# Performance work log

Hardware: AMD Instinct MI355X
Metric: run time of the kernel (lower is better)

## Reference

```python
import jax, jax.numpy as jnp
import numpy as np

# ---- sign binarization with straight-through estimator (standard BNN) ----
@jax.custom_vjp
def binarize(x):
    return jnp.where(x >= 0, 1.0, -1.0).astype(x.dtype)

def _bin_fwd(x):
    return binarize(x), x

def _bin_bwd(x, g):
    return (g * (jnp.abs(x) <= 1.0).astype(g.dtype),)

binarize.defvjp(_bin_fwd, _bin_bwd)

def conv2d(x, w):
    # x: [N,C,H,W], w: [O,I,kh,kw], stride 1, VALID padding (padding=0)
    return jax.lax.conv_general_dilated(
        x, w, window_strides=(1, 1), padding='VALID',
        dimension_numbers=('NCHW', 'OIHW', 'NCHW'))

def maxpool2(x):
    return jax.lax.reduce_window(x, -jnp.inf, jax.lax.max,
                                 (1, 1, 2, 2), (1, 1, 2, 2), 'VALID')

def hardtanh(x):
    return jnp.clip(x, -1.0, 1.0)

def setup_inputs() -> dict:
    key = jax.random.key(0)
    ks = jax.random.split(key, 11)
    B = 8192
    s = 0.1
    return {
        'x':   jax.random.normal(ks[0], (B, 3, 32, 32), jnp.float32),
        'w1':  jax.random.normal(ks[1], (6, 3, 5, 5), jnp.float32) * s,
        'b1':  jax.random.normal(ks[2], (6,), jnp.float32) * s,
        'w2':  jax.random.normal(ks[3], (16, 6, 5, 5), jnp.float32) * s,
        'b2':  jax.random.normal(ks[4], (16,), jnp.float32) * s,
        'wf1': jax.random.normal(ks[5], (120, 400), jnp.float32) * s,
        'bf1': jax.random.normal(ks[6], (120,), jnp.float32) * s,
        'wf2': jax.random.normal(ks[7], (84, 120), jnp.float32) * s,
        'bf2': jax.random.normal(ks[8], (84,), jnp.float32) * s,
        'wf3': jax.random.normal(ks[9], (10, 84), jnp.float32) * s,
        'bf3': jax.random.normal(ks[10], (10,), jnp.float32) * s,
    }

def reference(x, w1, b1, w2, b2, wf1, bf1, wf2, bf2, wf3, bf3):
    # conv1: first layer -> real-valued input, binarized weights
    out = conv2d(x, binarize(w1)) + b1[None, :, None, None]   # [B,6,28,28]
    out = maxpool2(hardtanh(out))                              # [B,6,14,14]
    # conv2: binarized input and weights
    out = conv2d(binarize(out), binarize(w2)) + b2[None, :, None, None]  # [B,16,10,10]
    out = maxpool2(hardtanh(out))                              # [B,16,5,5]
    out = out.reshape(out.shape[0], -1)                        # [B,400]
    out = hardtanh(binarize(out) @ binarize(wf1).T + bf1)      # [B,120]
    out = hardtanh(binarize(out) @ binarize(wf2).T + bf2)      # [B,84]
    out = binarize(out) @ binarize(wf3).T + bf3                # [B,10]
    return out
```

## Files before the change

kernel.cpp:

```cpp
#include <hip/hip_runtime.h>
#include <stdint.h>

#define TPB 64
#define RCAP 64
#define BAND 0.05f

#define WS_BFR   0
#define WS_W1B   1280
#define WS_W2PK  1298
#define WS_WF1P  1378
#define WS_WF2PK 4380
#define WS_WF3PK 4716
#define WS_T2    4746
#define WS_TF1   4762
#define WS_TF2   4882

typedef _Float16 half8 __attribute__((ext_vector_type(8)));
typedef float f32x4 __attribute__((ext_vector_type(4)));
typedef unsigned int u32x4 __attribute__((ext_vector_type(4)));

__device__ __forceinline__ uint32_t pkf16(float a, float b) {
  uint32_t lo = (uint32_t)__builtin_bit_cast(uint16_t, (_Float16)a);
  uint32_t hi = (uint32_t)__builtin_bit_cast(uint16_t, (_Float16)b);
  return lo | (hi << 16);
}

__device__ __forceinline__ float qpswap(float v) {
  return __builtin_bit_cast(float, __builtin_amdgcn_mov_dpp(
      __builtin_bit_cast(int, v), 0xB1, 0xF, 0xF, true));
}

__device__ __forceinline__ double win_sum(const float* __restrict__ xb,
                                          uint32_t b0, uint32_t b1, uint32_t b2) {
  double s = 0.0;
#pragma unroll
  for (int ic = 0; ic < 3; ++ic)
#pragma unroll
    for (int rr = 0; rr < 5; ++rr) {
      const float* rp = xb + ic * 1024 + rr * 32;
#pragma unroll
      for (int kc = 0; kc < 5; ++kc) {
        const int idx = ic * 25 + rr * 5 + kc;
        const uint32_t bw = (idx < 32) ? b0 : ((idx < 64) ? b1 : b2);
        double xv = (double)rp[kc];
        s += ((bw >> (idx & 31)) & 1u) ? xv : -xv;
      }
    }
  return s;
}

__global__ __launch_bounds__(256) void prep_kernel(
    const float* __restrict__ w1, const float* __restrict__ w2,
    const float* __restrict__ wf1, const float* __restrict__ wf2,
    const float* __restrict__ wf3,
    const float* __restrict__ b2, const float* __restrict__ bf1,
    const float* __restrict__ bf2, uint32_t* __restrict__ wsu)
{
  int id = blockIdx.x * 256 + threadIdx.x;
  if (id < 1280) {
    int s = id >> 8, r = id & 255, ln = r >> 2, dw = r & 3;
    int g4 = ln >> 4, n = ln & 15;
    int o = 4 * s + g4, r6 = o / 3, cp = o % 3;
    int c = n >> 1, dy = n & 1;
    uint32_t w = 0;
    for (int h = 0; h < 2; ++h) {
      int j2 = dw * 2 + h;
      int ic = j2 & 3, pix = j2 >> 2, kc = cp * 2 + pix, kr = r6 - dy;
      uint32_t f = 0;
      if (n < 12 && o < 18 && ic < 3 && kc < 5 && kr >= 0 && kr <= 4)
        f = (w1[(c * 3 + ic) * 25 + kr * 5 + kc] >= 0.f) ? 0x3C00u : 0xBC00u;
      w |= f << (16 * h);
    }
    wsu[WS_BFR + id] = w;
  } else if (id < 1298) {
    int i = id - 1280, c = i / 3, q = i % 3;
    uint32_t w = 0;
    for (int b = 0; b < 32; ++b) {
      int k = q * 32 + b;
      if (k < 75) w |= (uint32_t)(w1[c*75 + k] >= 0.f) << b;
    }
    wsu[WS_W1B + i] = w;
  } else if (id < 1378) {
    int r = id - 1298, oc = r / 5, kr = r % 5;
    uint32_t w = 0;
    for (int c = 0; c < 6; ++c)
      for (int k = 0; k < 5; ++k)
        w |= (uint32_t)(w2[((oc*6 + c)*5 + kr)*5 + k] >= 0.f) << (5*c + k);
    wsu[WS_W2PK + r] = w;
  } else if (id < 4378) {
    int r = id - 1378, o = r / 25, p = r % 25;
    uint32_t w = 0;
    for (int oc = 0; oc < 16; ++oc)
      w |= (uint32_t)(wf1[o*400 + oc*25 + p] >= 0.f) << oc;
    wsu[WS_WF1P + r] = w;
  } else if (id >= 4380 && id < 4716) {
    int r = id - 4380, o = r / 4, q = r % 4;
    uint32_t w = 0;
    for (int b = 0; b < 32; ++b) {
      int n = q*32 + b;
      if (n < 120) w |= (uint32_t)(wf2[o*120 + n] >= 0.f) << b;
    }
    wsu[WS_WF2PK + r] = w;
  } else if (id >= 4716 && id < 4746) {
    int r = id - 4716, o = r / 3, q = r % 3;
    uint32_t w = 0;
    for (int b = 0; b < 32; ++b) {
      int n = q*32 + b;
      if (n < 84) w |= (uint32_t)(wf3[o*84 + n] >= 0.f) << b;
    }
    wsu[WS_WF3PK + r] = w;
  } else if (id >= WS_T2 && id < WS_T2 + 16) {
    int oc = id - WS_T2, T = -1;
    for (int d = 0; d <= 150; ++d)
      if ((float)(150 - 2*d) + b2[oc] >= 0.f) T = d;
    wsu[id] = (uint32_t)T;
  } else if (id >= WS_TF1 && id < WS_TF1 + 120) {
    int o = id - WS_TF1, T = -1;
    for (int d = 0; d <= 400; ++d)
      if ((float)(400 - 2*d) + bf1[o] >= 0.f) T = d;
    wsu[id] = (uint32_t)T;
  } else if (id >= WS_TF2 && id < WS_TF2 + 84) {
    int o = id - WS_TF2, T = -1;
    for (int d = 0; d <= 120; ++d)
      if ((float)(120 - 2*d) + bf2[o] >= 0.f) T = d;
    wsu[id] = (uint32_t)T;
  }
}

__global__ void __launch_bounds__(TPB, 4) lenet_kernel(
    const float* __restrict__ x,
    const float* __restrict__ b1,
    const float* __restrict__ bf3,
    const uint32_t* __restrict__ wsu,
    float* __restrict__ out)
{
  __shared__ __align__(16) uint32_t imgh[2112];
  __shared__ uint32_t bits1[6][14];
  __shared__ uint32_t border_[6][14];
  __shared__ uint32_t bits2s[25];
  __shared__ uint32_t rlist[RCAP];
  __shared__ int rcnt;

  const int t = threadIdx.x;
  const int m16 = t & 15;
  const int g4 = t >> 4;
  const long long img = blockIdx.x;

  u32x4 bfr[5];
#pragma unroll
  for (int s = 0; s < 5; ++s)
    bfr[s] = *(const u32x4*)&wsu[WS_BFR + (s << 8) + (t << 2)];
  int koffs[5];
#pragma unroll
  for (int s = 0; s < 5; ++s) {
    const int o = 4 * s + g4;
    koffs[s] = (o < 18) ? (o / 3) * 33 + (o % 3) * 2 : 0;
  }

  {
    const int y = t >> 1, xh = t & 1;
    const float* rp = x + img * 3072 + y * 32 + xh * 16;
    const int pixbase = y * 33 + xh * 16;
#pragma unroll
    for (int q = 0; q < 4; ++q) {
      float4 f0 = *(const float4*)(rp +    0 + 4 * q);
      float4 f1 = *(const float4*)(rp + 1024 + 4 * q);
      float4 f2 = *(const float4*)(rp + 2048 + 4 * q);
      uint32_t* d = &imgh[2 * (pixbase + 4 * q)];
      *(uint2*)(d + 0) = make_uint2(pkf16(f0.x, f1.x), pkf16(f2.x, 0.f));
      *(uint2*)(d + 2) = make_uint2(pkf16(f0.y, f1.y), pkf16(f2.y, 0.f));
      *(uint2*)(d + 4) = make_uint2(pkf16(f0.z, f1.z), pkf16(f2.z, 0.f));
      *(uint2*)(d + 6) = make_uint2(pkf16(f0.w, f1.w), pkf16(f2.w, 0.f));
    }
    if (t < 32)
      *(uint2*)&imgh[2 * (t * 33 + 32)] = make_uint2(0u, 0u);
    if (t == 0) rcnt = 0;
  }
  __syncthreads();

  {
    const int n = m16;
    const int c = n >> 1;
    const float bcr = b1[(n < 12) ? c : 0];

    auto epilogue = [&](f32x4 aX, f32x4 aY, int pyi) {
      float pX0 = fmaxf(aX[0], aX[1]), pX1 = fmaxf(aX[2], aX[3]);
      float pY0 = fmaxf(aY[0], aY[1]), pY1 = fmaxf(aY[2], aY[3]);
      float qX0 = fmaxf(pX0, qpswap(pX0));
      float qX1 = fmaxf(pX1, qpswap(pX1));
      float qY0 = fmaxf(pY0, qpswap(pY0));
      float qY1 = fmaxf(pY1, qpswap(pY1));
      uint32_t comb = 0;
      {
        float v0 = qX0 + bcr, v1 = qX1 + bcr, v2 = qY0 + bcr, v3 = qY1 + bcr;
        const int p0 = g4 * 2, p1 = g4 * 2 + 1, p2 = 6 + g4 * 2, p3 = 7 + g4 * 2;
        if (fabsf(v0) < BAND) comb |= 1u << (16 + p0); else if (v0 >= 0.f) comb |= 1u << p0;
        if (fabsf(v1) < BAND) comb |= 1u << (16 + p1); else if (v1 >= 0.f) comb |= 1u << p1;
        if (fabsf(v2) < BAND) comb |= 1u << (16 + p2); else if (v2 >= 0.f) comb |= 1u << p2;
        if (fabsf(v3) < BAND) comb |= 1u << (16 + p3); else if (v3 >= 0.f) comb |= 1u << p3;
      }
      comb |= __shfl_xor(comb, 16);
      comb |= __shfl_xor(comb, 32);
      if (g4 == 0 && n < 12 && (n & 1) == 0) {
        bits1[c][pyi]   = comb & 0x3FFFu;
        border_[c][pyi] = comb >> 16;
      }
    };

    for (int p = 0; p < 7; ++p) {
      const int rpA = (2 * p) * 33 + m16;
      const int rpB = (2 * (p + 7)) * 33 + m16;
      f32x4 aX0 = {0.f,0.f,0.f,0.f}, aY0 = {0.f,0.f,0.f,0.f};
      f32x4 aX1 = {0.f,0.f,0.f,0.f}, aY1 = {0.f,0.f,0.f,0.f};
#pragma unroll
      for (int s = 0; s < 5; ++s) {
        const uint2* pX0 = (const uint2*)&imgh[2 * (rpA + koffs[s])];
        const uint2* pY0 = (const uint2*)&imgh[2 * (rpA + 12 + koffs[s])];
        const uint2* pX1 = (const uint2*)&imgh[2 * (rpB + koffs[s])];
        const uint2* pY1 = (const uint2*)&imgh[2 * (rpB + 12 + koffs[s])];
        uint2 a0 = pX0[0], a1 = pX0[1];
        uint2 b0 = pY0[0], b1_ = pY0[1];
        uint2 c0 = pX1[0], c1 = pX1[1];
        uint2 d0 = pY1[0], d1 = pY1[1];
        u32x4 wa = {a0.x, a0.y, a1.x, a1.y};
        u32x4 wb = {b0.x, b0.y, b1_.x, b1_.y};
        u32x4 wc = {c0.x, c0.y, c1.x, c1.y};
        u32x4 wd = {d0.x, d0.y, d1.x, d1.y};
        aX0 = __builtin_amdgcn_mfma_f32_16x16x32_f16(
                __builtin_bit_cast(half8, wa), __builtin_bit_cast(half8, bfr[s]), aX0, 0, 0, 0);
        aY0 = __builtin_amdgcn_mfma_f32_16x16x32_f16(
                __builtin_bit_cast(half8, wb), __builtin_bit_cast(half8, bfr[s]), aY0, 0, 0, 0);
        aX1 = __builtin_amdgcn_mfma_f32_16x16x32_f16(
                __builtin_bit_cast(half8, wc), __builtin_bit_cast(half8, bfr[s]), aX1, 0, 0, 0);
        aY1 = __builtin_amdgcn_mfma_f32_16x16x32_f16(
                __builtin_bit_cast(half8, wd), __builtin_bit_cast(half8, bfr[s]), aY1, 0, 0, 0);
      }
      epilogue(aX0, aY0, p);
      epilogue(aX1, aY1, p + 7);
    }
  }
  __syncthreads();

  for (int id = t; id < 84; id += TPB) {
    uint32_t bw = ((uint32_t*)border_)[id];
    while (bw) {
      int pj = __ffs(bw) - 1;
      bw &= bw - 1;
      int slot = atomicAdd(&rcnt, 1);
      if (slot < RCAP) rlist[slot] = (uint32_t)(id * 16 + pj);
    }
  }
  __syncthreads();

  {
    const int cnt = min(rcnt, RCAP);
    for (int k = t; k < cnt * 4; k += TPB) {
      const int e = k >> 2, win = k & 3;
      const uint32_t ent = rlist[e];
      const int pj = ent & 15, w = ent >> 4;
      const int pi = w % 14, c = w / 14;
      const int dr = win >> 1, dc = win & 1;
      const float* xb = x + img * 3072 + (2*pi + dr) * 32 + (2*pj + dc);
      double s = win_sum(xb, wsu[WS_W1B + c*3], wsu[WS_W1B + c*3+1], wsu[WS_W1B + c*3+2]);
      double s1 = fmax(s, __shfl_xor(s, 1));
      double sm = fmax(s1, __shfl_xor(s1, 2));
      if (win == 0) {
        if (sm + (double)b1[c] >= 0.0)
          atomicOr(&((uint32_t*)bits1)[w], 1u << pj);
      }
    }
    if (rcnt > RCAP) {
      for (int id = t; id < 1176; id += TPB) {
        const int w = id / 14, pj = id % 14;
        if ((((uint32_t*)border_)[w] >> pj) & 1u) {
          const int pi = w % 14, c = w / 14;
          double best = -1e300;
          for (int dr = 0; dr < 2; ++dr)
            for (int dc = 0; dc < 2; ++dc) {
              const float* xb = x + img * 3072 + (2*pi + dr) * 32 + (2*pj + dc);
              double s = win_sum(xb, wsu[WS_W1B + c*3], wsu[WS_W1B + c*3+1], wsu[WS_W1B + c*3+2]);
              best = best > s ? best : s;
            }
          if (best + (double)b1[c] >= 0.0)
            atomicOr(&((uint32_t*)bits1)[w], 1u << pj);
        }
      }
    }
  }
  __syncthreads();

  {
    const int la  = (t < 50) ? t : 49;
    const int i   = la / 5;
    const int pjc = la % 5;
    const int j0  = 2 * pjc;
    uint32_t ppA[5], ppB[5];
#pragma unroll
    for (int kr = 0; kr < 5; ++kr) {
      uint32_t wa = 0, wb = 0;
#pragma unroll
      for (int c = 0; c < 6; ++c) {
        uint32_t bc = bits1[c][i + kr];
        wa |= ((bc >> j0) & 31u) << (5*c);
        wb |= ((bc >> (j0 + 1)) & 31u) << (5*c);
      }
      ppA[kr] = wa; ppB[kr] = wb;
    }
    const int partner = (i & 1) ? (la - 5) : (la + 5);
    uint32_t myword = 0;
#pragma unroll 4
    for (int oc = 0; oc < 16; ++oc) {
      int dA = 0, dB = 0;
#pragma unroll
      for (int kr = 0; kr < 5; ++kr) {
        const uint32_t wv = wsu[WS_W2PK + oc*5 + kr];
        dA += __popc(ppA[kr] ^ wv);
        dB += __popc(ppB[kr] ^ wv);
      }
      int dm = min(dA, dB);
      int dp = __shfl(dm, partner);
      int dmin = min(dm, dp);
      myword |= (dmin <= (int)wsu[WS_T2 + oc] ? 1u : 0u) << oc;
    }
    if (t < 50 && (i & 1) == 0) bits2s[(i >> 1) * 5 + pjc] = myword;
  }
  __syncthreads();

  uint32_t f1w0, f1w1, f1w2, f1w3;
  {
    uint32_t p2[25];
#pragma unroll
    for (int p = 0; p < 25; ++p) p2[p] = bits2s[p];
    const uint32_t* wrA = wsu + WS_WF1P + t * 25;
    int d1 = 0;
#pragma unroll
    for (int p = 0; p < 25; ++p) d1 += __popc(p2[p] ^ wrA[p]);
    const bool act2 = (t < 56);
    const int o2 = 64 + t;
    int d2 = 0;
    const uint32_t* wrB = wsu + WS_WF1P + o2 * 25;
    if (act2) {
#pragma unroll
      for (int p = 0; p < 25; ++p) d2 += __popc(p2[p] ^ wrB[p]);
    }
    unsigned long long mA = __ballot(d1 <= (int)wsu[WS_TF1 + t]);
    unsigned long long mB = __ballot(act2 && (d2 <= (int)wsu[WS_TF1 + (act2 ? o2 : 0)]));
    f1w0 = (uint32_t)mA; f1w1 = (uint32_t)(mA >> 32);
    f1w2 = (uint32_t)mB; f1w3 = (uint32_t)(mB >> 32);
  }

  uint32_t f2w0, f2w1, f2w2;
  {
    const uint32_t* wr = wsu + WS_WF2PK + t * 4;
    int d3 = __popc(f1w0 ^ wr[0]) + __popc(f1w1 ^ wr[1]) +
             __popc(f1w2 ^ wr[2]) + __popc(f1w3 ^ wr[3]);
    const bool act4 = (t < 20);
    const int o4 = 64 + t;
    const uint32_t* wr2 = wsu + WS_WF2PK + (act4 ? o4 : 0) * 4;
    int d4 = 0;
    if (act4)
      d4 = __popc(f1w0 ^ wr2[0]) + __popc(f1w1 ^ wr2[1]) +
           __popc(f1w2 ^ wr2[2]) + __popc(f1w3 ^ wr2[3]);
    unsigned long long mC = __ballot((t < 84) && (d3 <= (int)wsu[WS_TF2 + ((t < 84) ? t : 0)]));
    unsigned long long mD = __ballot(act4 && (d4 <= (int)wsu[WS_TF2 + (act4 ? o4 : 0)]));
    f2w0 = (uint32_t)mC; f2w1 = (uint32_t)(mC >> 32); f2w2 = (uint32_t)mD;
  }

  if (t < 10) {
    int d = __popc(f2w0 ^ wsu[WS_WF3PK + t*3 + 0]) +
            __popc(f2w1 ^ wsu[WS_WF3PK + t*3 + 1]) +
            __popc(f2w2 ^ wsu[WS_WF3PK + t*3 + 2]);
    out[img*10 + t] = (float)(84 - 2*d) + bf3[t];
  }
}

extern "C" void kernel_launch(void* const* d_in, const int* in_sizes, int n_in,
                              void* d_out, int out_size, void* d_ws, size_t ws_size,
                              hipStream_t stream)
{
  const float* x   = (const float*)d_in[0];
  const float* w1  = (const float*)d_in[1];
  const float* b1  = (const float*)d_in[2];
  const float* w2  = (const float*)d_in[3];
  const float* b2  = (const float*)d_in[4];
  const float* wf1 = (const float*)d_in[5];
  const float* bf1 = (const float*)d_in[6];
  const float* wf2 = (const float*)d_in[7];
  const float* bf2 = (const float*)d_in[8];
  const float* wf3 = (const float*)d_in[9];
  const float* bf3 = (const float*)d_in[10];
  uint32_t* wsu = (uint32_t*)d_ws;

  const int imgs = in_sizes[0] / 3072;
  hipLaunchKernelGGL(prep_kernel, dim3(20), dim3(256), 0, stream,
                     w1, w2, wf1, wf2, wf3, b2, bf1, bf2, wsu);
  hipLaunchKernelGGL(lenet_kernel, dim3(imgs), dim3(TPB), 0, stream,
                     x, b1, bf3, wsu, (float*)d_out);
}
```

Baseline: 69.82 us.

## Pack four images per block and stream input rows through a ring buffer

Each 256-thread block now runs four wavefronts, one image each, and every wave has its own LDS slice. The input image is loaded in three row chunks into a 16-row ring buffer instead of being staged whole, which roughly halves LDS per image so more images fit per CU. The residual list capacity also shrinks. The cost is extra block-wide barriers between the chunks, which couple the four waves together, and a higher chance of falling back to the full border recompute path.

```diff
diff --git a/kernel.cpp b/kernel.cpp
--- a/kernel.cpp
+++ b/kernel.cpp
@@ -1,9 +1,10 @@
 #include <hip/hip_runtime.h>
 #include <stdint.h>
 
-#define TPB 64
-#define RCAP 64
+#define TPB 256
+#define RCAP 16
 #define BAND 0.05f
+#define SLICE 1268
 
 #define WS_BFR   0
 #define WS_W1B   1280
@@ -127,162 +128,160 @@
   }
 }
 
-__global__ void __launch_bounds__(TPB, 4) lenet_kernel(
+__global__ void __launch_bounds__(TPB, 8) lenet_kernel(
     const float* __restrict__ x,
     const float* __restrict__ b1,
     const float* __restrict__ bf3,
     const uint32_t* __restrict__ wsu,
-    float* __restrict__ out)
+    float* __restrict__ out, int imgs)
 {
-  __shared__ __align__(16) uint32_t imgh[2112];
-  __shared__ uint32_t bits1[6][14];
-  __shared__ uint32_t border_[6][14];
-  __shared__ uint32_t bits2s[25];
-  __shared__ uint32_t rlist[RCAP];
-  __shared__ int rcnt;
+  __shared__ __align__(16) uint32_t lds_all[4 * SLICE];
 
   const int t = threadIdx.x;
-  const int m16 = t & 15;
-  const int g4 = t >> 4;
-  const long long img = blockIdx.x;
+  const int lane = t & 63;
+  const int wv = t >> 6;
+  const int m16 = lane & 15;
+  const int g4 = lane >> 4;
+  long long img = (long long)blockIdx.x * 4 + wv;
+  if (img >= imgs) img = imgs - 1;
+
+  uint32_t* S       = lds_all + wv * SLICE;
+  uint32_t* s_img   = S;
+  uint32_t* s_bits1 = S + 1056;
+  uint32_t* s_bord  = S + 1140;
+  uint32_t* s_bits2 = S + 1224;
+  uint32_t* s_rlist = S + 1249;
+  uint32_t* s_rcnt  = S + 1265;
 
   u32x4 bfr[5];
 #pragma unroll
   for (int s = 0; s < 5; ++s)
-    bfr[s] = *(const u32x4*)&wsu[WS_BFR + (s << 8) + (t << 2)];
-  int koffs[5];
+    bfr[s] = *(const u32x4*)&wsu[WS_BFR + (s << 8) + (lane << 2)];
+  int r6s[5], cpos[5];
 #pragma unroll
   for (int s = 0; s < 5; ++s) {
     const int o = 4 * s + g4;
-    koffs[s] = (o < 18) ? (o / 3) * 33 + (o % 3) * 2 : 0;
-  }
-
-  {
-    const int y = t >> 1, xh = t & 1;
-    const float* rp = x + img * 3072 + y * 32 + xh * 16;
-    const int pixbase = y * 33 + xh * 16;
-#pragma unroll
-    for (int q = 0; q < 4; ++q) {
-      float4 f0 = *(const float4*)(rp +    0 + 4 * q);
-      float4 f1 = *(const float4*)(rp + 1024 + 4 * q);
-      float4 f2 = *(const float4*)(rp + 2048 + 4 * q);
-      uint32_t* d = &imgh[2 * (pixbase + 4 * q)];
+    if (o < 18) { r6s[s] = o / 3; cpos[s] = (o % 3) * 2 + m16; }
+    else        { r6s[s] = 0;     cpos[s] = 0; }
+  }
+
+  const float* xb = x + img * 3072;
+  auto load_rows = [&](int row0, int nrows) {
+    for (int id = lane; id < nrows * 8; id += 64) {
+      const int rr = row0 + (id >> 3), q = id & 7;
+      const float* rp = xb + rr * 32 + 4 * q;
+      float4 f0 = *(const float4*)(rp);
+      float4 f1 = *(const float4*)(rp + 1024);
+      float4 f2 = *(const float4*)(rp + 2048);
+      uint32_t* d = &s_img[(((rr & 15) * 33) + 4 * q) * 2];
       *(uint2*)(d + 0) = make_uint2(pkf16(f0.x, f1.x), pkf16(f2.x, 0.f));
       *(uint2*)(d + 2) = make_uint2(pkf16(f0.y, f1.y), pkf16(f2.y, 0.f));
       *(uint2*)(d + 4) = make_uint2(pkf16(f0.z, f1.z), pkf16(f2.z, 0.f));
       *(uint2*)(d + 6) = make_uint2(pkf16(f0.w, f1.w), pkf16(f2.w, 0.f));
     }
-    if (t < 32)
-      *(uint2*)&imgh[2 * (t * 33 + 32)] = make_uint2(0u, 0u);
-    if (t == 0) rcnt = 0;
-  }
-  __syncthreads();
-
-  {
-    const int n = m16;
-    const int c = n >> 1;
-    const float bcr = b1[(n < 12) ? c : 0];
-
-    auto epilogue = [&](f32x4 aX, f32x4 aY, int pyi) {
-      float pX0 = fmaxf(aX[0], aX[1]), pX1 = fmaxf(aX[2], aX[3]);
-      float pY0 = fmaxf(aY[0], aY[1]), pY1 = fmaxf(aY[2], aY[3]);
-      float qX0 = fmaxf(pX0, qpswap(pX0));
-      float qX1 = fmaxf(pX1, qpswap(pX1));
-      float qY0 = fmaxf(pY0, qpswap(pY0));
-      float qY1 = fmaxf(pY1, qpswap(pY1));
-      uint32_t comb = 0;
-      {
-        float v0 = qX0 + bcr, v1 = qX1 + bcr, v2 = qY0 + bcr, v3 = qY1 + bcr;
-        const int p0 = g4 * 2, p1 = g4 * 2 + 1, p2 = 6 + g4 * 2, p3 = 7 + g4 * 2;
-        if (fabsf(v0) < BAND) comb |= 1u << (16 + p0); else if (v0 >= 0.f) comb |= 1u << p0;
-        if (fabsf(v1) < BAND) comb |= 1u << (16 + p1); else if (v1 >= 0.f) comb |= 1u << p1;
-        if (fabsf(v2) < BAND) comb |= 1u << (16 + p2); else if (v2 >= 0.f) comb |= 1u << p2;
-        if (fabsf(v3) < BAND) comb |= 1u << (16 + p3); else if (v3 >= 0.f) comb |= 1u << p3;
-      }
-      comb |= __shfl_xor(comb, 16);
-      comb |= __shfl_xor(comb, 32);
-      if (g4 == 0 && n < 12 && (n & 1) == 0) {
-        bits1[c][pyi]   = comb & 0x3FFFu;
-        border_[c][pyi] = comb >> 16;
-      }
-    };
-
-    for (int p = 0; p < 7; ++p) {
-      const int rpA = (2 * p) * 33 + m16;
-      const int rpB = (2 * (p + 7)) * 33 + m16;
-      f32x4 aX0 = {0.f,0.f,0.f,0.f}, aY0 = {0.f,0.f,0.f,0.f};
-      f32x4 aX1 = {0.f,0.f,0.f,0.f}, aY1 = {0.f,0.f,0.f,0.f};
-#pragma unroll
-      for (int s = 0; s < 5; ++s) {
-        const uint2* pX0 = (const uint2*)&imgh[2 * (rpA + koffs[s])];
-        const uint2* pY0 = (const uint2*)&imgh[2 * (rpA + 12 + koffs[s])];
-        const uint2* pX1 = (const uint2*)&imgh[2 * (rpB + koffs[s])];
-        const uint2* pY1 = (const uint2*)&imgh[2 * (rpB + 12 + koffs[s])];
-        uint2 a0 = pX0[0], a1 = pX0[1];
-        uint2 b0 = pY0[0], b1_ = pY0[1];
-        uint2 c0 = pX1[0], c1 = pX1[1];
-        uint2 d0 = pY1[0], d1 = pY1[1];
-        u32x4 wa = {a0.x, a0.y, a1.x, a1.y};
-        u32x4 wb = {b0.x, b0.y, b1_.x, b1_.y};
-        u32x4 wc = {c0.x, c0.y, c1.x, c1.y};
-        u32x4 wd = {d0.x, d0.y, d1.x, d1.y};
-        aX0 = __builtin_amdgcn_mfma_f32_16x16x32_f16(
-                __builtin_bit_cast(half8, wa), __builtin_bit_cast(half8, bfr[s]), aX0, 0, 0, 0);
-        aY0 = __builtin_amdgcn_mfma_f32_16x16x32_f16(
-                __builtin_bit_cast(half8, wb), __builtin_bit_cast(half8, bfr[s]), aY0, 0, 0, 0);
-        aX1 = __builtin_amdgcn_mfma_f32_16x16x32_f16(
-                __builtin_bit_cast(half8, wc), __builtin_bit_cast(half8, bfr[s]), aX1, 0, 0, 0);
-        aY1 = __builtin_amdgcn_mfma_f32_16x16x32_f16(
-                __builtin_bit_cast(half8, wd), __builtin_bit_cast(half8, bfr[s]), aY1, 0, 0, 0);
-      }
-      epilogue(aX0, aY0, p);
-      epilogue(aX1, aY1, p + 7);
-    }
-  }
-  __syncthreads();
-
-  for (int id = t; id < 84; id += TPB) {
-    uint32_t bw = ((uint32_t*)border_)[id];
+  };
+
+  const int n = m16;
+  const int c = n >> 1;
+  const float bcr = b1[(n < 12) ? c : 0];
+  auto conv_row = [&](int pyi) {
+    f32x4 aX = {0.f,0.f,0.f,0.f}, aY = {0.f,0.f,0.f,0.f};
+#pragma unroll
+    for (int s = 0; s < 5; ++s) {
+      const int pix = ((2 * pyi + r6s[s]) & 15) * 33 + cpos[s];
+      const uint2* pX = (const uint2*)&s_img[2 * pix];
+      const uint2* pY = (const uint2*)&s_img[2 * (pix + 12)];
+      uint2 x0 = pX[0], x1 = pX[1];
+      uint2 y0 = pY[0], y1 = pY[1];
+      u32x4 wa = {x0.x, x0.y, x1.x, x1.y};
+      u32x4 wb = {y0.x, y0.y, y1.x, y1.y};
+      aX = __builtin_amdgcn_mfma_f32_16x16x32_f16(
+             __builtin_bit_cast(half8, wa), __builtin_bit_cast(half8, bfr[s]), aX, 0, 0, 0);
+      aY = __builtin_amdgcn_mfma_f32_16x16x32_f16(
+             __builtin_bit_cast(half8, wb), __builtin_bit_cast(half8, bfr[s]), aY, 0, 0, 0);
+    }
+    float pX0 = fmaxf(aX[0], aX[1]), pX1 = fmaxf(aX[2], aX[3]);
+    float pY0 = fmaxf(aY[0], aY[1]), pY1 = fmaxf(aY[2], aY[3]);
+    float qX0 = fmaxf(pX0, qpswap(pX0));
+    float qX1 = fmaxf(pX1, qpswap(pX1));
+    float qY0 = fmaxf(pY0, qpswap(pY0));
+    float qY1 = fmaxf(pY1, qpswap(pY1));
+    uint32_t comb = 0;
+    {
+      float v0 = qX0 + bcr, v1 = qX1 + bcr, v2 = qY0 + bcr, v3 = qY1 + bcr;
+      const int p0 = g4 * 2, p1 = g4 * 2 + 1, p2 = 6 + g4 * 2, p3 = 7 + g4 * 2;
+      if (fabsf(v0) < BAND) comb |= 1u << (16 + p0); else if (v0 >= 0.f) comb |= 1u << p0;
+      if (fabsf(v1) < BAND) comb |= 1u << (16 + p1); else if (v1 >= 0.f) comb |= 1u << p1;
+      if (fabsf(v2) < BAND) comb |= 1u << (16 + p2); else if (v2 >= 0.f) comb |= 1u << p2;
+      if (fabsf(v3) < BAND) comb |= 1u << (16 + p3); else if (v3 >= 0.f) comb |= 1u << p3;
+    }
+    comb |= __shfl_xor(comb, 16);
+    comb |= __shfl_xor(comb, 32);
+    if (g4 == 0 && n < 12 && (n & 1) == 0) {
+      s_bits1[c * 14 + pyi] = comb & 0x3FFFu;
+      s_bord [c * 14 + pyi] = comb >> 16;
+    }
+  };
+
+  if (lane == 0) *s_rcnt = 0;
+  load_rows(0, 16);
+  if (lane < 16)
+    *(uint2*)&s_img[(lane * 33 + 32) * 2] = make_uint2(0u, 0u);
+  __syncthreads();
+  for (int p = 0; p < 6; ++p) conv_row(p);
+  __syncthreads();
+  load_rows(16, 12);
+  __syncthreads();
+  for (int p = 6; p < 12; ++p) conv_row(p);
+  __syncthreads();
+  load_rows(28, 4);
+  __syncthreads();
+  conv_row(12); conv_row(13);
+  __syncthreads();
+
+  for (int id = lane; id < 84; id += 64) {
+    uint32_t bw = s_bord[id];
     while (bw) {
       int pj = __ffs(bw) - 1;
       bw &= bw - 1;
-      int slot = atomicAdd(&rcnt, 1);
-      if (slot < RCAP) rlist[slot] = (uint32_t)(id * 16 + pj);
+      int slot = atomicAdd((int*)s_rcnt, 1);
+      if (slot < RCAP) s_rlist[slot] = (uint32_t)(id * 16 + pj);
     }
   }
   __syncthreads();
 
   {
-    const int cnt = min(rcnt, RCAP);
-    for (int k = t; k < cnt * 4; k += TPB) {
+    const int rc = (int)*s_rcnt;
+    const int cnt = min(rc, RCAP);
+    for (int k = lane; k < cnt * 4; k += 64) {
       const int e = k >> 2, win = k & 3;
-      const uint32_t ent = rlist[e];
+      const uint32_t ent = s_rlist[e];
       const int pj = ent & 15, w = ent >> 4;
-      const int pi = w % 14, c = w / 14;
+      const int pi = w % 14, cc = w / 14;
       const int dr = win >> 1, dc = win & 1;
-      const float* xb = x + img * 3072 + (2*pi + dr) * 32 + (2*pj + dc);
-      double s = win_sum(xb, wsu[WS_W1B + c*3], wsu[WS_W1B + c*3+1], wsu[WS_W1B + c*3+2]);
+      const float* xw = xb + (2*pi + dr) * 32 + (2*pj + dc);
+      double s = win_sum(xw, wsu[WS_W1B + cc*3], wsu[WS_W1B + cc*3+1], wsu[WS_W1B + cc*3+2]);
       double s1 = fmax(s, __shfl_xor(s, 1));
       double sm = fmax(s1, __shfl_xor(s1, 2));
       if (win == 0) {
-        if (sm + (double)b1[c] >= 0.0)
-          atomicOr(&((uint32_t*)bits1)[w], 1u << pj);
-      }
-    }
-    if (rcnt > RCAP) {
-      for (int id = t; id < 1176; id += TPB) {
+        if (sm + (double)b1[cc] >= 0.0)
+          atomicOr(&s_bits1[w], 1u << pj);
+      }
+    }
+    if (rc > RCAP) {
+      for (int id = lane; id < 1176; id += 64) {
         const int w = id / 14, pj = id % 14;
-        if ((((uint32_t*)border_)[w] >> pj) & 1u) {
-          const int pi = w % 14, c = w / 14;
+        if ((s_bord[w] >> pj) & 1u) {
+          const int pi = w % 14, cc = w / 14;
           double best = -1e300;
           for (int dr = 0; dr < 2; ++dr)
             for (int dc = 0; dc < 2; ++dc) {
-              const float* xb = x + img * 3072 + (2*pi + dr) * 32 + (2*pj + dc);
-              double s = win_sum(xb, wsu[WS_W1B + c*3], wsu[WS_W1B + c*3+1], wsu[WS_W1B + c*3+2]);
+              const float* xw = xb + (2*pi + dr) * 32 + (2*pj + dc);
+              double s = win_sum(xw, wsu[WS_W1B + cc*3], wsu[WS_W1B + cc*3+1], wsu[WS_W1B + cc*3+2]);
               best = best > s ? best : s;
             }
-          if (best + (double)b1[c] >= 0.0)
-            atomicOr(&((uint32_t*)bits1)[w], 1u << pj);
+          if (best + (double)b1[cc] >= 0.0)
+            atomicOr(&s_bits1[w], 1u << pj);
         }
       }
     }
@@ -290,7 +289,7 @@
   __syncthreads();
 
   {
-    const int la  = (t < 50) ? t : 49;
+    const int la  = (lane < 50) ? lane : 49;
     const int i   = la / 5;
     const int pjc = la % 5;
     const int j0  = 2 * pjc;
@@ -299,10 +298,10 @@
     for (int kr = 0; kr < 5; ++kr) {
       uint32_t wa = 0, wb = 0;
 #pragma unroll
-      for (int c = 0; c < 6; ++c) {
-        uint32_t bc = bits1[c][i + kr];
-        wa |= ((bc >> j0) & 31u) << (5*c);
-        wb |= ((bc >> (j0 + 1)) & 31u) << (5*c);
+      for (int cc = 0; cc < 6; ++cc) {
+        uint32_t bc = s_bits1[cc * 14 + i + kr];
+        wa |= ((bc >> j0) & 31u) << (5*cc);
+        wb |= ((bc >> (j0 + 1)) & 31u) << (5*cc);
       }
       ppA[kr] = wa; ppB[kr] = wb;
     }
@@ -313,16 +312,16 @@
       int dA = 0, dB = 0;
 #pragma unroll
       for (int kr = 0; kr < 5; ++kr) {
-        const uint32_t wv = wsu[WS_W2PK + oc*5 + kr];
-        dA += __popc(ppA[kr] ^ wv);
-        dB += __popc(ppB[kr] ^ wv);
+        const uint32_t wv2 = wsu[WS_W2PK + oc*5 + kr];
+        dA += __popc(ppA[kr] ^ wv2);
+        dB += __popc(ppB[kr] ^ wv2);
       }
       int dm = min(dA, dB);
       int dp = __shfl(dm, partner);
       int dmin = min(dm, dp);
       myword |= (dmin <= (int)wsu[WS_T2 + oc] ? 1u : 0u) << oc;
     }
-    if (t < 50 && (i & 1) == 0) bits2s[(i >> 1) * 5 + pjc] = myword;
+    if (lane < 50 && (i & 1) == 0) s_bits2[(i >> 1) * 5 + pjc] = myword;
   }
   __syncthreads();
 
@@ -330,20 +329,20 @@
   {
     uint32_t p2[25];
 #pragma unroll
-    for (int p = 0; p < 25; ++p) p2[p] = bits2s[p];
-    const uint32_t* wrA = wsu + WS_WF1P + t * 25;
+    for (int p = 0; p < 25; ++p) p2[p] = s_bits2[p];
+    const uint32_t* wrA = wsu + WS_WF1P + lane * 25;
     int d1 = 0;
 #pragma unroll
     for (int p = 0; p < 25; ++p) d1 += __popc(p2[p] ^ wrA[p]);
-    const bool act2 = (t < 56);
-    const int o2 = 64 + t;
+    const bool act2 = (lane < 56);
+    const int o2 = 64 + lane;
     int d2 = 0;
     const uint32_t* wrB = wsu + WS_WF1P + o2 * 25;
     if (act2) {
 #pragma unroll
       for (int p = 0; p < 25; ++p) d2 += __popc(p2[p] ^ wrB[p]);
     }
-    unsigned long long mA = __ballot(d1 <= (int)wsu[WS_TF1 + t]);
+    unsigned long long mA = __ballot(d1 <= (int)wsu[WS_TF1 + lane]);
     unsigned long long mB = __ballot(act2 && (d2 <= (int)wsu[WS_TF1 + (act2 ? o2 : 0)]));
     f1w0 = (uint32_t)mA; f1w1 = (uint32_t)(mA >> 32);
     f1w2 = (uint32_t)mB; f1w3 = (uint32_t)(mB >> 32);
@@ -351,26 +350,26 @@
 
   uint32_t f2w0, f2w1, f2w2;
   {
-    const uint32_t* wr = wsu + WS_WF2PK + t * 4;
+    const uint32_t* wr = wsu + WS_WF2PK + lane * 4;
     int d3 = __popc(f1w0 ^ wr[0]) + __popc(f1w1 ^ wr[1]) +
              __popc(f1w2 ^ wr[2]) + __popc(f1w3 ^ wr[3]);
-    const bool act4 = (t < 20);
-    const int o4 = 64 + t;
+    const bool act4 = (lane < 20);
+    const int o4 = 64 + lane;
     const uint32_t* wr2 = wsu + WS_WF2PK + (act4 ? o4 : 0) * 4;
     int d4 = 0;
     if (act4)
       d4 = __popc(f1w0 ^ wr2[0]) + __popc(f1w1 ^ wr2[1]) +
            __popc(f1w2 ^ wr2[2]) + __popc(f1w3 ^ wr2[3]);
-    unsigned long long mC = __ballot((t < 84) && (d3 <= (int)wsu[WS_TF2 + ((t < 84) ? t : 0)]));
+    unsigned long long mC = __ballot(d3 <= (int)wsu[WS_TF2 + lane]);
     unsigned long long mD = __ballot(act4 && (d4 <= (int)wsu[WS_TF2 + (act4 ? o4 : 0)]));
     f2w0 = (uint32_t)mC; f2w1 = (uint32_t)(mC >> 32); f2w2 = (uint32_t)mD;
   }
 
-  if (t < 10) {
-    int d = __popc(f2w0 ^ wsu[WS_WF3PK + t*3 + 0]) +
-            __popc(f2w1 ^ wsu[WS_WF3PK + t*3 + 1]) +
-            __popc(f2w2 ^ wsu[WS_WF3PK + t*3 + 2]);
-    out[img*10 + t] = (float)(84 - 2*d) + bf3[t];
+  if (lane < 10) {
+    int d = __popc(f2w0 ^ wsu[WS_WF3PK + lane*3 + 0]) +
+            __popc(f2w1 ^ wsu[WS_WF3PK + lane*3 + 1]) +
+            __popc(f2w2 ^ wsu[WS_WF3PK + lane*3 + 2]);
+    out[img*10 + lane] = (float)(84 - 2*d) + bf3[lane];
   }
 }
 
@@ -394,6 +393,7 @@
   const int imgs = in_sizes[0] / 3072;
   hipLaunchKernelGGL(prep_kernel, dim3(20), dim3(256), 0, stream,
                      w1, w2, wf1, wf2, wf3, b2, bf1, bf2, wsu);
-  hipLaunchKernelGGL(lenet_kernel, dim3(imgs), dim3(TPB), 0, stream,
-                     x, b1, bf3, wsu, (float*)d_out);
-}
+  const int nblk = (imgs + 3) / 4;
+  hipLaunchKernelGGL(lenet_kernel, dim3(nblk), dim3(TPB), 0, stream,
+                     x, b1, bf3, wsu, (float*)d_out, imgs);
+}
```

After: 88.15 us. 1.26x slower.
